# Kernel tuning notes

Measured on AMD Instinct MI355X. Metric: run time of the kernel, lower is better.

The kernel has to match this reference:

```python
import jax, jax.numpy as jnp
import numpy as np
import math

SCALE = 16.0
IGNORE_THRES = 0.5
BAD_CONF_WEIGHT = 1.25
NB, NT, NA, NH, NW, NC = 16, 50, 5, 128, 128, 20


def _inv_tanh(y):
    ys = jnp.clip(y, -1.0 + 1e-6, 1.0 - 1e-6)
    at = 0.5 * jnp.log((1.0 + ys) / (1.0 - ys))
    return jnp.where(y <= -1.0, -2.0, jnp.where(y >= 1.0, 2.0, at))


def _forward(prediction, target, target_sizes, anchors):
    nB, nA, nH, nW, _ = prediction.shape
    nC = prediction.shape[-1] - 6
    s = SCALE
    # scaled anchors and anchor corner points (matches __init__ precompute)
    aw = anchors[:, 0] / s
    ah = anchors[:, 1] / s
    ar = anchors[:, 2]
    cr, sr = jnp.cos(ar), jnp.sin(ar)
    anchor_points = jnp.stack([-cr * aw, sr * aw, cr * aw, -sr * aw,
                               -sr * ah, -cr * ah, sr * ah, cr * ah], axis=1)  # [nA,8]
    anchor_hws = (ah + aw) / 2.0

    pred_conf = prediction[..., 0]
    x = prediction[..., 1]; y = prediction[..., 2]; r = prediction[..., 3]
    h = prediction[..., 4]; w = prediction[..., 5]
    pred_cls = prediction[..., 6:]

    # ---- build_targets_dist, vectorized (original uses detached .cpu().data) ----
    tgt = jax.lax.stop_gradient(target)
    T = tgt.shape[1]
    valid = jnp.arange(T)[None, :] < target_sizes[:, None]
    gx = tgt[..., 0] / s; gy = tgt[..., 1] / s
    gw = tgt[..., 4] / s; gh = tgt[..., 3] / s
    gr = tgt[..., 2]
    valid = valid & (gw != 0) & (gh != 0)
    gi = jnp.clip(gx.astype(jnp.int32), 0, nW - 1)
    gj = jnp.clip(gy.astype(jnp.int32), 0, nH - 1)
    pts = tgt[..., 5:13] / s
    cpts = pts - jnp.tile(jnp.stack([gx, gy], axis=-1), (1, 1, 4))  # centered corners [nB,T,8]
    deltas = cpts[:, :, None, :] - anchor_points[None, None, :, :]  # [nB,T,nA,8]
    dn = sum(jnp.linalg.norm(deltas[..., i:i + 2], axis=-1) for i in (0, 2, 4, 6))
    norm = (((gh + gw) / 2.0)[:, :, None] + anchor_hws[None, None, :]) / 2.0
    anch_dists = (dn / norm) ** 2  # [nB,T,nA]

    # conf_mask: zero anchors closer than ignore_thres at (gj,gi)
    conf_mask = jnp.ones((nB, nA, nH, nW), jnp.float32)
    b3 = jnp.broadcast_to(jnp.arange(nB)[:, None, None], (nB, T, nA)).reshape(-1)
    a3 = jnp.broadcast_to(jnp.arange(nA)[None, None, :], (nB, T, nA)).reshape(-1)
    gj3 = jnp.broadcast_to(gj[:, :, None], (nB, T, nA)).reshape(-1)
    gi3 = jnp.broadcast_to(gi[:, :, None], (nB, T, nA)).reshape(-1)
    ign = ((anch_dists < IGNORE_THRES) & valid[:, :, None]).reshape(-1)
    conf_mask = conf_mask.at[b3, a3, gj3, gi3].min(jnp.where(ign, 0.0, 1.0))

    best_n = jnp.argmin(anch_dists, axis=-1)  # [nB,T]
    txv = _inv_tanh(gx - (gi.astype(jnp.float32) + 0.5))
    tyv = _inv_tanh(gy - (gj.astype(jnp.float32) + 0.5))
    rd = gr - ar[best_n]
    rd = jnp.where(rd > math.pi, rd - 2 * math.pi,
                   jnp.where(rd < -math.pi, rd + 2 * math.pi, rd))
    trv = _inv_tanh(rd / (math.pi / 2))
    twv = jnp.log(gw / aw[best_n] + 1e-16)
    thv = jnp.log(gh / ah[best_n] + 1e-16)
    tlabv = jnp.argmax(tgt[..., 13:], axis=-1)

    bS = jnp.where(valid, jnp.arange(nB)[:, None], -1).reshape(-1)  # -1 -> dropped
    idx = (bS, best_n.reshape(-1), gj.reshape(-1), gi.reshape(-1))
    z = jnp.zeros((nB, nA, nH, nW), jnp.float32)
    mask = z.at[idx].set(1.0, mode='drop')
    conf_mask = conf_mask.at[idx].set(1.0, mode='drop')
    tx = z.at[idx].set(txv.reshape(-1), mode='drop')
    ty = z.at[idx].set(tyv.reshape(-1), mode='drop')
    tw = z.at[idx].set(twv.reshape(-1), mode='drop')
    th = z.at[idx].set(thv.reshape(-1), mode='drop')
    tr = z.at[idx].set(trv.reshape(-1), mode='drop')
    tconf = mask  # tconf set to 1 exactly where mask is 1
    tlab = jnp.zeros((nB, nA, nH, nW), jnp.int32).at[idx].set(
        tlabv.reshape(-1).astype(jnp.int32), mode='drop')

    conf_mask_false = conf_mask * (1.0 - mask)

    def masked_bce(z_, t_, m_):
        l = jnp.maximum(z_, 0.0) - z_ * t_ + jnp.log1p(jnp.exp(-jnp.abs(z_)))
        return jnp.sum(l * m_) / jnp.maximum(jnp.sum(m_), 1.0)

    def masked_mse(p_, t_):
        return jnp.sum(((p_ - t_) ** 2) * mask) / jnp.maximum(jnp.sum(mask), 1.0)

    loss_conf = BAD_CONF_WEIGHT * masked_bce(pred_conf, tconf, conf_mask_false) \
        + masked_bce(pred_conf, tconf, mask)
    loss_x = masked_mse(x, tx); loss_y = masked_mse(y, ty)
    loss_w = masked_mse(w, tw); loss_h = masked_mse(h, th)
    loss_r = masked_mse(r, tr)
    logp = jax.nn.log_softmax(pred_cls, axis=-1)
    nll = -jnp.take_along_axis(logp, tlab[..., None], axis=-1)[..., 0]
    loss_cls = jnp.sum(nll * mask) / jnp.maximum(jnp.sum(mask), 1.0)
    return loss_x + loss_y + loss_w + loss_h + loss_r + loss_conf + loss_cls


def setup_inputs():
    key = jax.random.key(0)
    ks = jax.random.split(key, 8)
    s = SCALE
    prediction = jax.random.normal(ks[0], (NB, NA, NH, NW, 6 + NC), jnp.float32) * 0.5
    # targets in image pixel space (grid is NHxNW at stride SCALE)
    cx = jax.random.uniform(ks[1], (NB, NT), minval=1.0, maxval=NW - 1.0) * s
    cy = jax.random.uniform(ks[2], (NB, NT), minval=1.0, maxval=NH - 1.0) * s
    bw = jax.random.uniform(ks[3], (NB, NT), minval=8.0, maxval=96.0)
    bh = jax.random.uniform(ks[4], (NB, NT), minval=8.0, maxval=48.0)
    br = jax.random.uniform(ks[5], (NB, NT), minval=-0.3, maxval=0.3)
    c, si = jnp.cos(br), jnp.sin(br)
    pts = jnp.stack([cx - c * bw, cy + si * bw, cx + c * bw, cy - si * bw,
                     cx - si * bh, cy - c * bh, cx + si * bh, cy + c * bh], axis=-1)
    cls = jax.nn.one_hot(jax.random.randint(ks[6], (NB, NT), 0, NC), NC, dtype=jnp.float32)
    target = jnp.concatenate([jnp.stack([cx, cy, br, bh, bw], axis=-1), pts, cls], axis=-1)
    target_sizes = jax.random.randint(ks[7], (NB,), 20, NT + 1).astype(jnp.int32)
    anchors = jnp.array([[48., 16., 0.], [96., 24., 0.], [192., 32., 0.],
                         [64., 64., 0.], [32., 96., 1.5708]], jnp.float32)
    return {"prediction": prediction, "target": target,
            "target_sizes": target_sizes, "anchors": anchors}


def reference(prediction, target, target_sizes, anchors):
    return _forward(prediction, target, target_sizes, anchors)
```

## Files before the change

kernel.cpp:

```cpp
#include <hip/hip_runtime.h>
#include <math.h>

#define NBb 16
#define NTt 50
#define NAa 5
#define NHh 128
#define NWw 128
#define NCc 20
#define NCH 26
#define NCELL (NBb*NAa*NHh*NWw)
#define NREC  (NBb*NTt)
#define NLIST (NREC*7)
#define SCALE_F 16.0f
#define IGNORE_THRES_F 0.5f
#define BAD_CONF_WEIGHT_F 1.25f
#define PI_F 3.14159265358979323846f

#define STATUS_OFF 16
#define REC_OFF  (STATUS_OFF + NCELL)
#define LIST_OFF (REC_OFF + 6*NREC)

#define MAIN_GRID 1024
#define MAIN_BLK  256
#define MAIN_STRIDE (MAIN_GRID*MAIN_BLK)
static_assert(NCELL == 5 * MAIN_STRIDE, "conf loop unroll assumes 5 cells/thread");
static_assert(((STATUS_OFF + NCELL) & 3) == 0, "k_zero uint4 alignment");

__device__ __forceinline__ float inv_tanh_f(float y) {
  if (y <= -1.0f) return -2.0f;
  if (y >= 1.0f)  return  2.0f;
  float ys = fminf(fmaxf(y, -1.0f + 1e-6f), 1.0f - 1e-6f);
  return 0.5f * logf((1.0f + ys) / (1.0f - ys));
}

__device__ __forceinline__ float softplus_f(float z) {
  return fmaxf(z, 0.0f) + log1pf(expf(-fabsf(z)));
}

__global__ void k_zero(uint4* __restrict__ ws4) {
  const int n4 = (STATUS_OFF + NCELL) / 4;
  int stride = gridDim.x * blockDim.x;
  for (int i = blockIdx.x * blockDim.x + threadIdx.x; i < n4; i += stride)
    ws4[i] = make_uint4(0u, 0u, 0u, 0u);
}

__global__ void k_prep(const float* __restrict__ tgt,
                       const int* __restrict__ tsz,
                       const float* __restrict__ anch,
                       float* __restrict__ ws) {
  int tid = blockIdx.x * blockDim.x + threadIdx.x;
  if (tid >= NREC) return;
  int b = tid / NTt, t = tid % NTt;

  float aw[NAa], ah[NAa], ar[NAa], ahw[NAa], ap[NAa][8];
  for (int a = 0; a < NAa; ++a) {
    aw[a] = anch[a*3+0] / SCALE_F;
    ah[a] = anch[a*3+1] / SCALE_F;
    ar[a] = anch[a*3+2];
    float cr = cosf(ar[a]), sr = sinf(ar[a]);
    ap[a][0] = -cr*aw[a]; ap[a][1] =  sr*aw[a];
    ap[a][2] =  cr*aw[a]; ap[a][3] = -sr*aw[a];
    ap[a][4] = -sr*ah[a]; ap[a][5] = -cr*ah[a];
    ap[a][6] =  sr*ah[a]; ap[a][7] =  cr*ah[a];
    ahw[a] = (ah[a] + aw[a]) * 0.5f;
  }

  const float* row = tgt + (size_t)tid * (13 + NCc);
  float gx = row[0] / SCALE_F;
  float gy = row[1] / SCALE_F;
  float gr = row[2];
  float gh = row[3] / SCALE_F;
  float gw = row[4] / SCALE_F;
  bool valid = (t < tsz[b]) && (gw != 0.0f) && (gh != 0.0f);
  if (!valid) return;

  int gi = (int)gx; gi = min(max(gi, 0), NWw - 1);
  int gj = (int)gy; gj = min(max(gj, 0), NHh - 1);

  float cp[8];
  for (int k = 0; k < 8; ++k)
    cp[k] = row[5 + k] / SCALE_F - ((k & 1) ? gy : gx);

  float bestd = 1e30f; int best = 0; unsigned ignm = 0;
  for (int a = 0; a < NAa; ++a) {
    float dn = 0.0f;
    for (int p = 0; p < 8; p += 2) {
      float dx = cp[p]   - ap[a][p];
      float dy = cp[p+1] - ap[a][p+1];
      dn += sqrtf(dx*dx + dy*dy);
    }
    float nm = ((gh + gw) * 0.5f + ahw[a]) * 0.5f;
    float d = dn / nm; d = d * d;
    if (d < IGNORE_THRES_F) ignm |= (1u << a);
    if (d < bestd) { bestd = d; best = a; }
  }

  unsigned* wsu = (unsigned*)ws;
  unsigned* status = wsu + STATUS_OFF;
  unsigned* list = wsu + LIST_OFF;
  int cellbase = ((b * NAa) * NHh + gj) * NWw + gi;
  for (int a = 0; a < NAa; ++a)
    if ((ignm >> a) & 1u) {
      int cell = cellbase + a * NHh * NWw;
      atomicMax(&status[cell], 1u);
      unsigned slot = atomicAdd(&wsu[15], 1u);
      list[slot] = (unsigned)cell;
    }
  {
    int cell = cellbase + best * NHh * NWw;
    atomicMax(&status[cell], 2u + (unsigned)tid);
    if (!((ignm >> best) & 1u)) {
      unsigned slot = atomicAdd(&wsu[15], 1u);
      list[slot] = (unsigned)cell;
    }
  }

  float txv = inv_tanh_f(gx - ((float)gi + 0.5f));
  float tyv = inv_tanh_f(gy - ((float)gj + 0.5f));
  float rd = gr - ar[best];
  if (rd > PI_F) rd -= 2.0f * PI_F;
  else if (rd < -PI_F) rd += 2.0f * PI_F;
  float trv = inv_tanh_f(rd / (PI_F * 0.5f));
  float twv = logf(gw / aw[best] + 1e-16f);
  float thv = logf(gh / ah[best] + 1e-16f);
  int tlab = 0; float bm = row[13];
  for (int c = 1; c < NCc; ++c)
    if (row[13 + c] > bm) { bm = row[13 + c]; tlab = c; }

  float* rec = ws + REC_OFF;
  rec[0*NREC + tid] = txv;
  rec[1*NREC + tid] = tyv;
  rec[2*NREC + tid] = twv;
  rec[3*NREC + tid] = thv;
  rec[4*NREC + tid] = trv;
  ((int*)rec)[5*NREC + tid] = tlab;
}

__global__ void __launch_bounds__(MAIN_BLK) k_main(const float* __restrict__ pred,
                                                   float* __restrict__ ws) {
  unsigned* wsu = (unsigned*)ws;
  unsigned* status = wsu + STATUS_OFF;
  const unsigned* list = wsu + LIST_OFF;
  const float* rec = ws + REC_OFF;
  int nlist = (int)wsu[15];
  int t = blockIdx.x * MAIN_BLK + threadIdx.x;

  float acc = 0.0f;
  #pragma unroll
  for (int k = 0; k < 5; ++k) {
    float z = pred[(size_t)(t + k * MAIN_STRIDE) * NCH];
    acc += softplus_f(z);
  }

  float sub = 0.0f, cnb = 0.0f, obj = 0.0f;
  float sx = 0.0f, sy = 0.0f, sw = 0.0f, sh = 0.0f, sr = 0.0f;
  float scls = 0.0f, cm = 0.0f;

  for (int i = t; i < nlist; i += MAIN_STRIDE) {
    unsigned cell = list[i];
    unsigned st = atomicExch(&status[cell], 0u);
    if (st == 0u) continue;
    const float* cp = pred + (size_t)cell * NCH;
    float z = cp[0];
    sub += softplus_f(z);
    cnb += 1.0f;
    if (st >= 2u) {
      int r = (int)(st - 2u);
      obj += softplus_f(z) - z;
      float dx = cp[1] - rec[0*NREC + r];
      float dy = cp[2] - rec[1*NREC + r];
      float dr = cp[3] - rec[4*NREC + r];
      float dh = cp[4] - rec[3*NREC + r];
      float dw = cp[5] - rec[2*NREC + r];
      sx += dx*dx; sy += dy*dy; sw += dw*dw; sh += dh*dh; sr += dr*dr;
      int tlab = ((const int*)rec)[5*NREC + r];
      float m = cp[6];
      for (int c = 1; c < NCc; ++c) m = fmaxf(m, cp[6 + c]);
      float s = 0.0f;
      for (int c = 0; c < NCc; ++c) s += expf(cp[6 + c] - m);
      scls += (m + logf(s)) - cp[6 + tlab];
      cm += 1.0f;
    }
  }

  float vals[11] = {acc, sub, cnb, obj, sx, sy, sw, sh, sr, scls, cm};
  __shared__ float red[4][11];
  int wid = threadIdx.x >> 6, lane = threadIdx.x & 63;
  #pragma unroll
  for (int k = 0; k < 11; ++k) {
    float v = vals[k];
    for (int off = 32; off; off >>= 1) v += __shfl_down(v, off, 64);
    if (lane == 0) red[wid][k] = v;
  }
  __syncthreads();
  if (threadIdx.x < 11) {
    float v = red[0][threadIdx.x] + red[1][threadIdx.x]
            + red[2][threadIdx.x] + red[3][threadIdx.x];
    if (v != 0.0f) atomicAdd(ws + threadIdx.x, v);
  }
}

__global__ void k_fin(const float* __restrict__ ws, float* __restrict__ out) {
  if (threadIdx.x == 0) {
    float acc = ws[0], sub = ws[1], cnb = ws[2], obj = ws[3];
    float sx = ws[4], sy = ws[5], sw = ws[6], sh = ws[7], sr = ws[8];
    float scls = ws[9], cm = ws[10];
    float acc_bg = acc - sub;
    float cnt_bg = (float)NCELL - cnb;
    float db = fmaxf(cnt_bg, 1.0f);
    float dm = fmaxf(cm, 1.0f);
    float loss_conf = BAD_CONF_WEIGHT_F * (acc_bg / db) + obj / dm;
    out[0] = (sx + sy + sw + sh + sr + scls) / dm + loss_conf;
  }
}

extern "C" void kernel_launch(void* const* d_in, const int* in_sizes, int n_in,
                              void* d_out, int out_size, void* d_ws, size_t ws_size,
                              hipStream_t stream) {
  const float* pred = (const float*)d_in[0];
  const float* tgt  = (const float*)d_in[1];
  const int*   tsz  = (const int*)d_in[2];
  const float* anch = (const float*)d_in[3];
  float* ws = (float*)d_ws;

  k_zero<<<320, 256, 0, stream>>>((uint4*)ws);
  k_prep<<<4, 256, 0, stream>>>(tgt, tsz, anch, ws);
  k_main<<<MAIN_GRID, MAIN_BLK, 0, stream>>>(pred, ws);
  k_fin<<<1, 64, 0, stream>>>(ws, (float*)d_out);
}
```

Before: 215.3 us.

## Drop status zeroing via self-describing marks and fuse finalize into main kernel

Removes the full-workspace zeroing kernel. Status cells now hold recognizable mark values set by a CAS loop, so stale or garbage contents never need clearing. The shared atomic list counter is replaced by fixed per-record list slots, and the finalize kernel is folded into k_main with a last-block-done pattern over 16 partial accumulator copies. The main grid is doubled with a launch-bounds occupancy hint. The intent is to save a roughly 5 MB memset and two kernel launches, at the cost of extra threadfence and atomic traffic and reliance on mark values never appearing in stale data.

```diff
diff --git a/kernel.cpp b/kernel.cpp
--- a/kernel.cpp
+++ b/kernel.cpp
@@ -10,21 +10,38 @@
 #define NCH 26
 #define NCELL (NBb*NAa*NHh*NWw)
 #define NREC  (NBb*NTt)
-#define NLIST (NREC*7)
+#define NSLOT 6
+#define NLIST (NREC*NSLOT)
 #define SCALE_F 16.0f
 #define IGNORE_THRES_F 0.5f
 #define BAD_CONF_WEIGHT_F 1.25f
 #define PI_F 3.14159265358979323846f
 
-#define STATUS_OFF 16
-#define REC_OFF  (STATUS_OFF + NCELL)
-#define LIST_OFF (REC_OFF + 6*NREC)
-
-#define MAIN_GRID 1024
-#define MAIN_BLK  256
-#define MAIN_STRIDE (MAIN_GRID*MAIN_BLK)
-static_assert(NCELL == 5 * MAIN_STRIDE, "conf loop unroll assumes 5 cells/thread");
-static_assert(((STATUS_OFF + NCELL) & 3) == 0, "k_zero uint4 alignment");
+#define DONE_IDX 12
+#define NCOPY 16
+#define ACC_OFF 16
+#define REC_OFF 272
+#define LIST_OFF 5072
+#define STATUS_OFF 16384
+
+#define MARK_IGN 0x7FFFFFFFu
+#define MARK_MASK_BASE 0x3FFFFFFFu
+#define CLAIMED 0xFFFFFFFFu
+
+__device__ __forceinline__ bool is_mark(unsigned u) {
+  return (u >= (MARK_MASK_BASE - (NREC - 1)) && u <= MARK_MASK_BASE) || (u == MARK_IGN);
+}
+
+__device__ __forceinline__ void mark_cell(unsigned* addr, unsigned val) {
+  unsigned cur = *addr;
+  while (true) {
+    unsigned desired = is_mark(cur) ? (cur < val ? cur : val) : val;
+    if (desired == cur) break;
+    unsigned old = atomicCAS(addr, cur, desired);
+    if (old == cur) break;
+    cur = old;
+  }
+}
 
 __device__ __forceinline__ float inv_tanh_f(float y) {
   if (y <= -1.0f) return -2.0f;
@@ -37,19 +54,19 @@
   return fmaxf(z, 0.0f) + log1pf(expf(-fabsf(z)));
 }
 
-__global__ void k_zero(uint4* __restrict__ ws4) {
-  const int n4 = (STATUS_OFF + NCELL) / 4;
-  int stride = gridDim.x * blockDim.x;
-  for (int i = blockIdx.x * blockDim.x + threadIdx.x; i < n4; i += stride)
-    ws4[i] = make_uint4(0u, 0u, 0u, 0u);
-}
-
 __global__ void k_prep(const float* __restrict__ tgt,
                        const int* __restrict__ tsz,
                        const float* __restrict__ anch,
                        float* __restrict__ ws) {
   int tid = blockIdx.x * blockDim.x + threadIdx.x;
+  unsigned* wsu = (unsigned*)ws;
+  if (tid < ACC_OFF + NCOPY*16) wsu[tid] = 0u;
   if (tid >= NREC) return;
+
+  unsigned* list = wsu + LIST_OFF;
+  #pragma unroll
+  for (int s = 0; s < NSLOT; ++s) list[tid*NSLOT + s] = CLAIMED;
+
   int b = tid / NTt, t = tid % NTt;
 
   float aw[NAa], ah[NAa], ar[NAa], ahw[NAa], ap[NAa][8];
@@ -95,24 +112,20 @@
     if (d < bestd) { bestd = d; best = a; }
   }
 
-  unsigned* wsu = (unsigned*)ws;
   unsigned* status = wsu + STATUS_OFF;
-  unsigned* list = wsu + LIST_OFF;
   int cellbase = ((b * NAa) * NHh + gj) * NWw + gi;
+  int nslot = 0;
   for (int a = 0; a < NAa; ++a)
     if ((ignm >> a) & 1u) {
       int cell = cellbase + a * NHh * NWw;
-      atomicMax(&status[cell], 1u);
-      unsigned slot = atomicAdd(&wsu[15], 1u);
-      list[slot] = (unsigned)cell;
+      mark_cell(&status[cell], MARK_IGN);
+      list[tid*NSLOT + nslot++] = (unsigned)cell;
     }
   {
     int cell = cellbase + best * NHh * NWw;
-    atomicMax(&status[cell], 2u + (unsigned)tid);
-    if (!((ignm >> best) & 1u)) {
-      unsigned slot = atomicAdd(&wsu[15], 1u);
-      list[slot] = (unsigned)cell;
-    }
+    mark_cell(&status[cell], MARK_MASK_BASE - (unsigned)tid);
+    if (!((ignm >> best) & 1u))
+      list[tid*NSLOT + nslot++] = (unsigned)cell;
   }
 
   float txv = inv_tanh_f(gx - ((float)gi + 0.5f));
@@ -136,50 +149,58 @@
   ((int*)rec)[5*NREC + tid] = tlab;
 }
 
-__global__ void __launch_bounds__(MAIN_BLK) k_main(const float* __restrict__ pred,
-                                                   float* __restrict__ ws) {
+#define MAIN_GRID 2048
+#define MAIN_BLK  256
+#define MAIN_THREADS (MAIN_GRID*MAIN_BLK)
+static_assert(2*MAIN_THREADS <= NCELL && 3*MAIN_THREADS >= NCELL, "phase-1 tiling");
+
+__global__ void __launch_bounds__(MAIN_BLK, 4) k_main(const float* __restrict__ pred,
+                                                      float* __restrict__ ws,
+                                                      float* __restrict__ out) {
   unsigned* wsu = (unsigned*)ws;
   unsigned* status = wsu + STATUS_OFF;
   const unsigned* list = wsu + LIST_OFF;
   const float* rec = ws + REC_OFF;
-  int nlist = (int)wsu[15];
   int t = blockIdx.x * MAIN_BLK + threadIdx.x;
 
-  float acc = 0.0f;
-  #pragma unroll
-  for (int k = 0; k < 5; ++k) {
-    float z = pred[(size_t)(t + k * MAIN_STRIDE) * NCH];
-    acc += softplus_f(z);
-  }
+  float z0 = pred[(size_t)t * NCH];
+  float z1 = pred[(size_t)(t + MAIN_THREADS) * NCH];
+  bool h2 = t < (NCELL - 2*MAIN_THREADS);
+  float z2 = h2 ? pred[(size_t)(t + 2*MAIN_THREADS) * NCH] : 0.0f;
+  float acc = softplus_f(z0) + softplus_f(z1);
+  if (h2) acc += softplus_f(z2);
 
   float sub = 0.0f, cnb = 0.0f, obj = 0.0f;
   float sx = 0.0f, sy = 0.0f, sw = 0.0f, sh = 0.0f, sr = 0.0f;
   float scls = 0.0f, cm = 0.0f;
 
-  for (int i = t; i < nlist; i += MAIN_STRIDE) {
-    unsigned cell = list[i];
-    unsigned st = atomicExch(&status[cell], 0u);
-    if (st == 0u) continue;
-    const float* cp = pred + (size_t)cell * NCH;
-    float z = cp[0];
-    sub += softplus_f(z);
-    cnb += 1.0f;
-    if (st >= 2u) {
-      int r = (int)(st - 2u);
-      obj += softplus_f(z) - z;
-      float dx = cp[1] - rec[0*NREC + r];
-      float dy = cp[2] - rec[1*NREC + r];
-      float dr = cp[3] - rec[4*NREC + r];
-      float dh = cp[4] - rec[3*NREC + r];
-      float dw = cp[5] - rec[2*NREC + r];
-      sx += dx*dx; sy += dy*dy; sw += dw*dw; sh += dh*dh; sr += dr*dr;
-      int tlab = ((const int*)rec)[5*NREC + r];
-      float m = cp[6];
-      for (int c = 1; c < NCc; ++c) m = fmaxf(m, cp[6 + c]);
-      float s = 0.0f;
-      for (int c = 0; c < NCc; ++c) s += expf(cp[6 + c] - m);
-      scls += (m + logf(s)) - cp[6 + tlab];
-      cm += 1.0f;
+  if (t < NLIST) {
+    unsigned cell = list[t];
+    if (cell < (unsigned)NCELL) {
+      unsigned st = atomicExch(&status[cell], CLAIMED);
+      if (is_mark(st)) {
+        const float* cpt = pred + (size_t)cell * NCH;
+        float z = cpt[0];
+        sub = softplus_f(z);
+        cnb = 1.0f;
+        if (st != MARK_IGN) {
+          int r = (int)(MARK_MASK_BASE - st);
+          obj = softplus_f(z) - z;
+          float dx = cpt[1] - rec[0*NREC + r];
+          float dy = cpt[2] - rec[1*NREC + r];
+          float dr = cpt[3] - rec[4*NREC + r];
+          float dh = cpt[4] - rec[3*NREC + r];
+          float dw = cpt[5] - rec[2*NREC + r];
+          sx = dx*dx; sy = dy*dy; sw = dw*dw; sh = dh*dh; sr = dr*dr;
+          int tlab = ((const int*)rec)[5*NREC + r];
+          float m = cpt[6];
+          for (int c = 1; c < NCc; ++c) m = fmaxf(m, cpt[6 + c]);
+          float s = 0.0f;
+          for (int c = 0; c < NCc; ++c) s += expf(cpt[6 + c] - m);
+          scls = (m + logf(s)) - cpt[6 + tlab];
+          cm = 1.0f;
+        }
+      }
     }
   }
 
@@ -193,24 +214,43 @@
     if (lane == 0) red[wid][k] = v;
   }
   __syncthreads();
+  int copy = blockIdx.x & (NCOPY - 1);
   if (threadIdx.x < 11) {
     float v = red[0][threadIdx.x] + red[1][threadIdx.x]
             + red[2][threadIdx.x] + red[3][threadIdx.x];
-    if (v != 0.0f) atomicAdd(ws + threadIdx.x, v);
-  }
-}
-
-__global__ void k_fin(const float* __restrict__ ws, float* __restrict__ out) {
+    if (v != 0.0f) atomicAdd(&ws[ACC_OFF + copy*16 + threadIdx.x], v);
+  }
+
+  __threadfence();
+  __syncthreads();
+  __shared__ int lastFlag;
   if (threadIdx.x == 0) {
-    float acc = ws[0], sub = ws[1], cnb = ws[2], obj = ws[3];
-    float sx = ws[4], sy = ws[5], sw = ws[6], sh = ws[7], sr = ws[8];
-    float scls = ws[9], cm = ws[10];
-    float acc_bg = acc - sub;
-    float cnt_bg = (float)NCELL - cnb;
+    unsigned old = atomicAdd(&wsu[DONE_IDX], 1u);
+    lastFlag = (old == MAIN_GRID - 1) ? 1 : 0;
+  }
+  __syncthreads();
+  if (!lastFlag) return;
+
+  __shared__ float part[NCOPY][11];
+  if (threadIdx.x < NCOPY*11) {
+    int c = threadIdx.x / 11, k = threadIdx.x % 11;
+    part[c][k] = atomicAdd(&ws[ACC_OFF + c*16 + k], 0.0f);
+  }
+  __syncthreads();
+  if (threadIdx.x == 0) {
+    float tot[11];
+    #pragma unroll
+    for (int k = 0; k < 11; ++k) {
+      float v = 0.0f;
+      for (int c = 0; c < NCOPY; ++c) v += part[c][k];
+      tot[k] = v;
+    }
+    float acc_bg = tot[0] - tot[1];
+    float cnt_bg = (float)NCELL - tot[2];
     float db = fmaxf(cnt_bg, 1.0f);
-    float dm = fmaxf(cm, 1.0f);
-    float loss_conf = BAD_CONF_WEIGHT_F * (acc_bg / db) + obj / dm;
-    out[0] = (sx + sy + sw + sh + sr + scls) / dm + loss_conf;
+    float dm = fmaxf(tot[10], 1.0f);
+    float loss_conf = BAD_CONF_WEIGHT_F * (acc_bg / db) + tot[3] / dm;
+    out[0] = (tot[4] + tot[5] + tot[6] + tot[7] + tot[8] + tot[9]) / dm + loss_conf;
   }
 }
 
@@ -223,8 +263,6 @@
   const float* anch = (const float*)d_in[3];
   float* ws = (float*)d_ws;
 
-  k_zero<<<320, 256, 0, stream>>>((uint4*)ws);
   k_prep<<<4, 256, 0, stream>>>(tgt, tsz, anch, ws);
-  k_main<<<MAIN_GRID, MAIN_BLK, 0, stream>>>(pred, ws);
-  k_fin<<<1, 64, 0, stream>>>(ws, (float*)d_out);
-}
+  k_main<<<MAIN_GRID, MAIN_BLK, 0, stream>>>(pred, ws, (float*)d_out);
+}
```

After: 474.2 us. +120.3%, slower.
